# Kernel tuning notes

Measured on AMD Instinct MI355X. Metric: run time of the kernel, lower is better.

## Reference

```python
import math
import jax, jax.numpy as jnp
import numpy as np

WS = 8      # window_size
NT = 16     # n_theta
NR = 8      # n_r
PD = 32     # polar_proj_dim


def _polar_grid():
    # Matches LocalPolarPrior._build_polar_grid: [NR, NT, 2] with (x, y) in [-1, 1]
    radius = jnp.linspace(0.0, 1.0, NR)
    theta = jnp.linspace(0.0, 2.0 * math.pi, NT + 1)[:-1]
    rr, tt = jnp.meshgrid(radius, theta, indexing='ij')
    return jnp.stack([rr * jnp.cos(tt), rr * jnp.sin(tt)], axis=-1)


def _bilinear_weights():
    # Precompute flat gather indices + weights for F.grid_sample(mode='bilinear',
    # padding_mode='zeros', align_corners=True) on a fixed WSxWS input.
    g = _polar_grid()                                   # [NR, NT, 2]
    px = (g[..., 0] + 1.0) * 0.5 * (WS - 1)             # x -> pixel coords
    py = (g[..., 1] + 1.0) * 0.5 * (WS - 1)
    x0 = jnp.floor(px); y0 = jnp.floor(py)
    wx = px - x0; wy = py - y0
    xs = jnp.stack([x0, x0 + 1, x0, x0 + 1], axis=-1)   # [NR, NT, 4]
    ys = jnp.stack([y0, y0, y0 + 1, y0 + 1], axis=-1)
    ws = jnp.stack([(1 - wx) * (1 - wy), wx * (1 - wy),
                    (1 - wx) * wy, wx * wy], axis=-1)
    valid = (xs >= 0) & (xs < WS) & (ys >= 0) & (ys < WS)
    xi = jnp.clip(xs, 0, WS - 1).astype(jnp.int32)
    yi = jnp.clip(ys, 0, WS - 1).astype(jnp.int32)
    idx = (yi * WS + xi).reshape(NR * NT, 4)            # flat [0, 64)
    wt = (ws * valid).reshape(NR * NT, 4).astype(jnp.float32)
    return idx, wt


def setup_inputs() -> dict:
    key = jax.random.key(0)
    k1, k2, k3 = jax.random.split(key, 3)
    x = jax.random.normal(k1, (8, 96, 384, 384), jnp.float32)
    W_proj = jax.random.normal(k2, (PD, 96), jnp.float32) * 0.1
    b_proj = jax.random.normal(k3, (PD,), jnp.float32) * 0.1
    return {"x": x, "W_proj": W_proj, "b_proj": b_proj}


def reference(x, W_proj, b_proj):
    B, C, H, W = x.shape
    hg, wg = H // WS, W // WS
    # 1x1 conv projection
    feat = jnp.einsum('bchw,oc->bohw', x, W_proj) + b_proj[None, :, None, None]
    # window partition -> [B*hg*wg, PD, WS, WS]
    win = (feat.reshape(B, PD, hg, WS, wg, WS)
               .transpose(0, 2, 4, 1, 3, 5)
               .reshape(B * hg * wg, PD, WS, WS))
    # per-window orthonormal FFT2, shift, log-magnitude
    spec = jnp.fft.fftshift(jnp.fft.fft2(win, norm='ortho'), axes=(-2, -1))
    mag = jnp.log1p(jnp.abs(spec))                      # [N, PD, WS, WS]
    # fixed bilinear polar resample (data-independent weights)
    idx, wt = _bilinear_weights()                       # [NR*NT, 4]
    magf = mag.reshape(-1, PD, WS * WS)
    samp = magf[:, :, idx]                              # [N, PD, NR*NT, 4]
    polar = (samp * wt).sum(-1).reshape(-1, PD, NR, NT)
    # direction distribution per window
    logits = polar.mean(axis=(1, 2))                    # [N, NT]
    dist = jax.nn.softmax(logits, axis=-1)
    d_local = dist.reshape(B, hg, wg, NT).transpose(0, 3, 1, 2)
    entropy = -(d_local * jnp.log(jnp.clip(d_local, 1e-8))).sum(axis=1, keepdims=True)
    confidence = jnp.clip(1.0 - entropy / math.log(NT), 0.0, 1.0)
    return d_local.astype(x.dtype), confidence.astype(x.dtype)
```

## Files before the change

### kernel.cpp

```cpp
#include <hip/hip_runtime.h>
#include <hip/hip_bf16.h>
#include <math.h>

#define NT 16
#define NR 8
#define PD 32
#define HG 48
#define WG 48
#define NB 8
#define CH 96
#define HW 384
#define XHW (HW * HW)
#define S8 0.70710678118654752f

typedef short short8 __attribute__((ext_vector_type(8)));
typedef float f32x4 __attribute__((ext_vector_type(4)));

static __device__ const float CT16[16] = {
    1.0f, 0.9238795325112867f, 0.7071067811865476f, 0.3826834323650898f,
    0.0f, -0.3826834323650898f, -0.7071067811865476f, -0.9238795325112867f,
    -1.0f, -0.9238795325112867f, -0.7071067811865476f, -0.3826834323650898f,
    0.0f, 0.3826834323650898f, 0.7071067811865476f, 0.9238795325112867f};
static __device__ const float ST16[16] = {
    0.0f, 0.3826834323650898f, 0.7071067811865476f, 0.9238795325112867f,
    1.0f, 0.9238795325112867f, 0.7071067811865476f, 0.3826834323650898f,
    0.0f, -0.3826834323650898f, -0.7071067811865476f, -0.9238795325112867f,
    -1.0f, -0.9238795325112867f, -0.7071067811865476f, -0.3826834323650898f};

static __device__ __forceinline__ unsigned short f2bf(float f) {
  unsigned int u = __float_as_uint(f);
  u = u + 0x7fffu + ((u >> 16) & 1u);
  return (unsigned short)(u >> 16);
}
static __device__ __forceinline__ unsigned int pk2bf(float a, float b) {
  union { __hip_bfloat162 h; unsigned int u; } c;
  c.h = __float22bfloat162_rn(make_float2(a, b));
  return c.u;
}
static __device__ __forceinline__ float bf2f_lo(unsigned int v) {
  return __uint_as_float(v << 16);
}
static __device__ __forceinline__ float bf2f_hi(unsigned int v) {
  return __uint_as_float(v & 0xffff0000u);
}

#define MAGR(x_) log1pf(0.125f * fabsf(x_))
#define MAGC(re_, im_) log1pf(0.125f * sqrtf((re_) * (re_) + (im_) * (im_)))

__global__ void lpp_setup(const float* __restrict__ Wp,
                          unsigned short* __restrict__ ws) {
  int gt = blockIdx.x * 256 + threadIdx.x;
  if (gt < 384) {
    int f = gt >> 6, l = gt & 63;
    int ks = f >> 1, nt = f & 1;
    int n = nt * 16 + (l & 15);
    int kbase = ks * 32 + (l >> 4) * 8;
    for (int jj = 0; jj < 8; ++jj)
      ws[(f * 64 + l) * 8 + jj] = f2bf(Wp[n * CH + kbase + jj]);
  }
  if (gt >= 1024 && gt < 2048) {
    int q = gt - 1024;
    int j = q >> 4, t = q & 15;
    float g = 0.f;
    for (int r = 0; r < 8; ++r) {
      float rad = (float)r / 7.0f;
      float px = (rad * CT16[t] + 1.0f) * 3.5f;
      float py = (rad * ST16[t] + 1.0f) * 3.5f;
      float xf = floorf(px), yf = floorf(py);
      float wx = px - xf, wy = py - yf;
      int ix = (int)xf, iy = (int)yf;
      int xi0 = min(max(ix, 0), 7), xi1 = min(max(ix + 1, 0), 7);
      int yi0 = min(max(iy, 0), 7), yi1 = min(max(iy + 1, 0), 7);
      bool vx0 = (ix >= 0) && (ix < 8), vx1 = (ix + 1 >= 0) && (ix + 1 < 8);
      bool vy0 = (iy >= 0) && (iy < 8), vy1 = (iy + 1 >= 0) && (iy + 1 < 8);
      float w0 = (vx0 && vy0) ? (1.f - wx) * (1.f - wy) : 0.f;
      float w1 = (vx1 && vy0) ? wx * (1.f - wy) : 0.f;
      float w2 = (vx0 && vy1) ? (1.f - wx) * wy : 0.f;
      float w3 = (vx1 && vy1) ? wx * wy : 0.f;
      if (yi0 * 8 + xi0 == j) g += w0;
      if (yi0 * 8 + xi1 == j) g += w1;
      if (yi1 * 8 + xi0 == j) g += w2;
      if (yi1 * 8 + xi1 == j) g += w3;
    }
    int f = j >> 5, kc = (j >> 3) & 3, jj = j & 7;
    int l = (kc << 4) | t;
    ws[3072 + (f * 64 + l) * 8 + jj] = f2bf(g);
  }
}

__global__ __launch_bounds__(256, 4) void lpp_main(
    const float* __restrict__ x, const float* __restrict__ bp,
    const unsigned short* __restrict__ ws, float* __restrict__ out) {
  __shared__ short8 ldsX[2048];
  __shared__ float obuf[144];
  unsigned int* ldsU = (unsigned int*)ldsX;

  const int tid = threadIdx.x;
  const int lane = tid & 63;
  const int wave = tid >> 6;
  const int gid = blockIdx.x;
  const int wxg = gid % 6;
  const int hy = (gid / 6) % HG;
  const int b = gid / (6 * HG);
  const short8* wsV = (const short8*)ws;
  const int kcA = lane >> 4;

  f32x4 acc[8][2];
#pragma unroll
  for (int m = 0; m < 8; ++m) {
    acc[m][0] = (f32x4){0.f, 0.f, 0.f, 0.f};
    acc[m][1] = (f32x4){0.f, 0.f, 0.f, 0.f};
  }

  short8 bfr[6];
#pragma unroll
  for (int f = 0; f < 6; ++f) bfr[f] = wsV[f * 64 + lane];

  const int pw = wave * 128 + (lane & 15);
  const float* tb = x + (size_t)b * CH * XHW + (size_t)(hy * 8) * HW +
                    wxg * 64 + (size_t)(kcA * 8) * XHW;

  float lv[2][8];
#define LOADSTEP(DST, S)                                                     \
  {                                                                          \
    int px_ = pw + ((S) & 7) * 16;                                           \
    int pxo_ = (px_ >> 6) * HW + (px_ & 63);                                 \
    _Pragma("unroll") for (int j = 0; j < 8; ++j)                            \
        DST[j] = tb[(size_t)(((S) >> 3) * 32 + j) * XHW + pxo_];             \
  }

  LOADSTEP(lv[0], 0)
#pragma unroll
  for (int s = 0; s < 24; ++s) {
    if (s + 1 < 24) LOADSTEP(lv[(s + 1) & 1], s + 1)
    union { unsigned int u[4]; short8 v; } pk;
    pk.u[0] = pk2bf(lv[s & 1][0], lv[s & 1][1]);
    pk.u[1] = pk2bf(lv[s & 1][2], lv[s & 1][3]);
    pk.u[2] = pk2bf(lv[s & 1][4], lv[s & 1][5]);
    pk.u[3] = pk2bf(lv[s & 1][6], lv[s & 1][7]);
    acc[s & 7][0] = __builtin_amdgcn_mfma_f32_16x16x32_bf16(
        pk.v, bfr[(s >> 3) * 2 + 0], acc[s & 7][0], 0, 0, 0);
    acc[s & 7][1] = __builtin_amdgcn_mfma_f32_16x16x32_bf16(
        pk.v, bfr[(s >> 3) * 2 + 1], acc[s & 7][1], 0, 0, 0);
  }

  {
    const float bias0 = bp[lane & 15];
    const float bias1 = bp[16 + (lane & 15)];
    const int r_ = 2 * wave;
    const int c0 = ((lane >> 4) & 1) << 2;
    const int wb = (lane >> 5) & 1;
#pragma unroll
    for (int m = 0; m < 8; ++m) {
      int win = (2 * m + wb) & 7;
      int j0 = (r_ + (m >> 2)) * 8 + c0;
#pragma unroll
      for (int nt = 0; nt < 2; ++nt) {
        int p = win * 32 + nt * 16 + (lane & 15);
        float bs = nt ? bias1 : bias0;
        int sh = (p & 15) << 1;
        int dwb = p * 32;
        unsigned int w0 = pk2bf(acc[m][nt][0] + bs, acc[m][nt][1] + bs);
        unsigned int w1 = pk2bf(acc[m][nt][2] + bs, acc[m][nt][3] + bs);
        ldsU[dwb + ((j0 >> 1) ^ sh)] = w0;
        ldsU[dwb + (((j0 >> 1) + 1) ^ sh)] = w1;
      }
    }
  }
  __syncthreads();

  {
    const int p = tid;
    const int sh = (p & 15) << 1;
    const int dwb = p * 32;
    float rr[8][8];
#pragma unroll
    for (int k = 0; k < 8; ++k) {
      float v[8];
#pragma unroll
      for (int i = 0; i < 4; ++i) {
        unsigned int u = ldsU[dwb + ((k * 4 + i) ^ sh)];
        v[2 * i] = bf2f_lo(u);
        v[2 * i + 1] = bf2f_hi(u);
      }
      float a0 = v[0] + v[4], a1 = v[0] - v[4], a2 = v[2] + v[6], a3 = v[2] - v[6];
      float b0 = v[1] + v[5], b1 = v[1] - v[5], b2 = v[3] + v[7], b3 = v[3] - v[7];
      float e0 = a0 + a2, e2 = a0 - a2, o0 = b0 + b2, o2 = b0 - b2;
      float t1 = S8 * (b1 - b3), t2 = S8 * (b1 + b3);
      rr[k][0] = e0 + o0; rr[k][1] = e0 - o0;
      rr[k][2] = a1 + t1; rr[k][3] = -a3 - t2;
      rr[k][4] = e2;      rr[k][5] = -o2;
      rr[k][6] = a1 - t1; rr[k][7] = a3 - t2;
    }
    float mg0[5], mg4[5], mg1[8], mg2[8], mg3[8];
#define REALCOL(SLOT, OUT)                                                    \
  {                                                                           \
    float a0 = rr[0][SLOT] + rr[4][SLOT], a1 = rr[0][SLOT] - rr[4][SLOT];     \
    float a2 = rr[2][SLOT] + rr[6][SLOT], a3 = rr[2][SLOT] - rr[6][SLOT];     \
    float b0 = rr[1][SLOT] + rr[5][SLOT], b1 = rr[1][SLOT] - rr[5][SLOT];     \
    float b2 = rr[3][SLOT] + rr[7][SLOT], b3 = rr[3][SLOT] - rr[7][SLOT];     \
    float e0 = a0 + a2, e2 = a0 - a2, o0 = b0 + b2, o2 = b0 - b2;             \
    float t1 = S8 * (b1 - b3), t2 = S8 * (b1 + b3);                           \
    OUT[0] = MAGR(e0 + o0); OUT[4] = MAGR(e0 - o0);                           \
    OUT[1] = MAGC(a1 + t1, -a3 - t2);                                         \
    OUT[2] = MAGC(e2, -o2);                                                   \
    OUT[3] = MAGC(a1 - t1, a3 - t2);                                          \
  }
#define CPLXCOL(SR, SI, OUT)                                                  \
  {                                                                           \
    float t0r = rr[0][SR] + rr[4][SR], t0i = rr[0][SI] + rr[4][SI];           \
    float t1r = rr[0][SR] - rr[4][SR], t1i = rr[0][SI] - rr[4][SI];           \
    float t2r = rr[2][SR] + rr[6][SR], t2i = rr[2][SI] + rr[6][SI];           \
    float t3r = rr[2][SR] - rr[6][SR], t3i = rr[2][SI] - rr[6][SI];           \
    float E0r = t0r + t2r, E0i = t0i + t2i, E2r = t0r - t2r, E2i = t0i - t2i; \
    float E1r = t1r + t3i, E1i = t1i - t3r, E3r = t1r - t3i, E3i = t1i + t3r; \
    float u0r = rr[1][SR] + rr[5][SR], u0i = rr[1][SI] + rr[5][SI];           \
    float u1r = rr[1][SR] - rr[5][SR], u1i = rr[1][SI] - rr[5][SI];           \
    float u2r = rr[3][SR] + rr[7][SR], u2i = rr[3][SI] + rr[7][SI];           \
    float u3r = rr[3][SR] - rr[7][SR], u3i = rr[3][SI] - rr[7][SI];           \
    float O0r = u0r + u2r, O0i = u0i + u2i, O2r = u0r - u2r, O2i = u0i - u2i; \
    float O1r = u1r + u3i, O1i = u1i - u3r, O3r = u1r - u3i, O3i = u1i + u3r; \
    float W1r = S8 * (O1r + O1i), W1i = S8 * (O1i - O1r);                     \
    float W2r = O2i, W2i = -O2r;                                              \
    float W3r = S8 * (O3i - O3r), W3i = -S8 * (O3r + O3i);                    \
    OUT[0] = MAGC(E0r + O0r, E0i + O0i); OUT[4] = MAGC(E0r - O0r, E0i - O0i); \
    OUT[1] = MAGC(E1r + W1r, E1i + W1i); OUT[5] = MAGC(E1r - W1r, E1i - W1i); \
    OUT[2] = MAGC(E2r + W2r, E2i + W2i); OUT[6] = MAGC(E2r - W2r, E2i - W2i); \
    OUT[3] = MAGC(E3r + W3r, E3i + W3i); OUT[7] = MAGC(E3r - W3r, E3i - W3i); \
  }
    REALCOL(0, mg0)
    REALCOL(1, mg4)
    CPLXCOL(2, 3, mg1)
    CPLXCOL(4, 5, mg2)
    CPLXCOL(6, 7, mg3)
    const int pb8 = p * 8, p7 = p & 7;
#pragma unroll
    for (int up = 0; up < 8; ++up) {
      union { unsigned short h[8]; short8 v; } pk;
#pragma unroll
      for (int vp = 0; vp < 8; ++vp) {
        const int u = (up + 4) & 7, vx = (vp + 4) & 7;
        float m;
        if (vx == 0)      m = mg0[(u <= 4) ? u : (8 - u)];
        else if (vx == 4) m = mg4[(u <= 4) ? u : (8 - u)];
        else if (vx == 1) m = mg1[u];
        else if (vx == 2) m = mg2[u];
        else if (vx == 3) m = mg3[u];
        else { const int uu = (8 - u) & 7;
               m = (vx == 5) ? mg3[uu] : (vx == 6) ? mg2[uu] : mg1[uu]; }
        pk.h[vp] = f2bf(m);
      }
      ldsX[pb8 + (up ^ p7)] = pk.v;
    }
  }
  __syncthreads();

  {
    short8 gf0 = wsV[384 + lane];
    short8 gf1 = wsV[448 + lane];
    f32x4 ag[4];
#pragma unroll
    for (int pt = 0; pt < 4; ++pt) {
      int prow = (wave * 4 + pt) * 16 + (lane & 15);
      int p7 = prow & 7, pb = prow * 8;
      short8 a0 = ldsX[pb + (kcA ^ p7)];
      short8 a1 = ldsX[pb + ((kcA + 4) ^ p7)];
      f32x4 zf = (f32x4){0.f, 0.f, 0.f, 0.f};
      zf = __builtin_amdgcn_mfma_f32_16x16x32_bf16(a0, gf0, zf, 0, 0, 0);
      zf = __builtin_amdgcn_mfma_f32_16x16x32_bf16(a1, gf1, zf, 0, 0, 0);
      ag[pt] = zf;
    }
    float s0 = ag[0][0] + ag[0][1] + ag[0][2] + ag[0][3] +
               ag[1][0] + ag[1][1] + ag[1][2] + ag[1][3];
    float s1 = ag[2][0] + ag[2][1] + ag[2][2] + ag[2][3] +
               ag[3][0] + ag[3][1] + ag[3][2] + ag[3][3];
    s0 += __shfl_xor(s0, 16); s0 += __shfl_xor(s0, 32);
    s1 += __shfl_xor(s1, 16); s1 += __shfl_xor(s1, 32);
    float l0 = s0 * (1.0f / 256.0f), l1 = s1 * (1.0f / 256.0f);
    float m0 = l0, m1 = l1;
#pragma unroll
    for (int mk = 1; mk < 16; mk <<= 1) {
      m0 = fmaxf(m0, __shfl_xor(m0, mk));
      m1 = fmaxf(m1, __shfl_xor(m1, mk));
    }
    float e0 = expf(l0 - m0), e1 = expf(l1 - m1);
    float ss0 = e0, ss1 = e1;
#pragma unroll
    for (int mk = 1; mk < 16; mk <<= 1) {
      ss0 += __shfl_xor(ss0, mk);
      ss1 += __shfl_xor(ss1, mk);
    }
    float d0 = e0 / ss0, d1 = e1 / ss1;
    float h0 = -d0 * logf(fmaxf(d0, 1e-8f));
    float h1 = -d1 * logf(fmaxf(d1, 1e-8f));
#pragma unroll
    for (int mk = 1; mk < 16; mk <<= 1) {
      h0 += __shfl_xor(h0, mk);
      h1 += __shfl_xor(h1, mk);
    }
    float c0 = fminf(fmaxf(1.f - h0 * (1.0f / 2.7725887222397811f), 0.f), 1.f);
    float c1 = fminf(fmaxf(1.f - h1 * (1.0f / 2.7725887222397811f), 0.f), 1.f);
    if (lane < 16) {
      obuf[wave * 32 + lane] = d0;
      obuf[wave * 32 + 16 + lane] = d1;
    }
    if (lane == 0) {
      obuf[128 + wave * 2] = c0;
      obuf[128 + wave * 2 + 1] = c1;
    }
  }
  __syncthreads();

  if (tid < 128) {
    int t = tid >> 3, win = tid & 7;
    int wx = wxg * 8 + win;
    out[((size_t)(b * NT + t) * HG + hy) * WG + wx] = obuf[win * 16 + t];
  } else if (tid < 136) {
    int win = tid - 128;
    int wx = wxg * 8 + win;
    out[(size_t)NB * NT * HG * WG + ((size_t)b * HG + hy) * WG + wx] =
        obuf[128 + win];
  }
}

extern "C" void kernel_launch(void* const* d_in, const int* in_sizes, int n_in,
                              void* d_out, int out_size, void* d_ws,
                              size_t ws_size, hipStream_t stream) {
  (void)in_sizes; (void)n_in; (void)ws_size; (void)out_size;
  const float* x = (const float*)d_in[0];
  const float* Wp = (const float*)d_in[1];
  const float* bp = (const float*)d_in[2];
  unsigned short* ws = (unsigned short*)d_ws;
  float* out = (float*)d_out;
  lpp_setup<<<8, 256, 0, stream>>>(Wp, ws);
  lpp_main<<<NB * HG * 6, 256, 0, stream>>>(x, bp, ws, out);
}
```

Measured before the change: 137.7 us.

## Split fused projection+FFT kernel into separate projection and FFT kernels via workspace

Splits the single fused kernel into two. A projection kernel streams full 384-pixel rows of x through bf16 MFMA and writes the bias-added features to global workspace in bf16. A second kernel then reads those features per window and does the FFT, polar resample and softmax. The aim is more coalesced, row-contiguous reads of x and less register pressure per kernel. The cost is an extra global write and read of the intermediate feature map, about 75 MB in bf16, plus one more launch.

```diff
diff --git a/kernel.cpp b/kernel.cpp
--- a/kernel.cpp
+++ b/kernel.cpp
@@ -12,6 +12,7 @@
 #define HW 384
 #define XHW (HW * HW)
 #define S8 0.70710678118654752f
+#define FEAT0 8192
 
 typedef short short8 __attribute__((ext_vector_type(8)));
 typedef float f32x4 __attribute__((ext_vector_type(4)));
@@ -88,12 +89,81 @@
   }
 }
 
-__global__ __launch_bounds__(256, 4) void lpp_main(
+__global__ __launch_bounds__(256, 4) void lpp_proj(
     const float* __restrict__ x, const float* __restrict__ bp,
+    const unsigned short* __restrict__ wsc, unsigned short* __restrict__ wsf) {
+  const int tid = threadIdx.x;
+  const int lane = tid & 63;
+  const int l15 = lane & 15;
+  const int kcA = lane >> 4;
+  const int w = tid >> 6;
+  const int gid = blockIdx.x;
+  const int rh = gid & 1;
+  const int hy = (gid >> 1) % HG;
+  const int b = gid / (2 * HG);
+  const int R = hy * 8 + rh * 4 + w;
+  const int Rw = rh * 4 + w;
+  const short8* wsV = (const short8*)wsc;
+
+  short8 bfr[6];
+#pragma unroll
+  for (int f = 0; f < 6; ++f) bfr[f] = wsV[f * 64 + lane];
+  const float bs0 = bp[l15];
+  const float bs1 = bp[16 + l15];
+
+  const float* xr = x + (size_t)b * CH * XHW + (size_t)R * HW +
+                    (size_t)(kcA * 8) * XHW;
+  const int FB0 = FEAT0 + ((b * HG + hy) * 48 * 8 + Rw) * 256;
+  const int colw = (kcA & 1) << 2;
+  const int wsel = kcA >> 1;
+
+  float laA[24], laB[24];
+#define K1LOAD(DST, M)                                                       \
+  {                                                                          \
+    _Pragma("unroll") for (int ks = 0; ks < 3; ++ks)                         \
+        _Pragma("unroll") for (int j = 0; j < 8; ++j)                        \
+            DST[ks * 8 + j] =                                                \
+                xr[(size_t)(ks * 32 + j) * XHW + (M) * 16 + l15];            \
+  }
+#define K1BODY(CUR, NXT, M)                                                  \
+  {                                                                          \
+    if ((M) + 1 < 24) K1LOAD(NXT, (M) + 1);                                  \
+    f32x4 a0 = (f32x4){0.f, 0.f, 0.f, 0.f};                                  \
+    f32x4 a1 = (f32x4){0.f, 0.f, 0.f, 0.f};                                  \
+    _Pragma("unroll") for (int ks = 0; ks < 3; ++ks) {                       \
+      union { unsigned int u[4]; short8 v; } pk;                             \
+      pk.u[0] = pk2bf(CUR[ks * 8 + 0], CUR[ks * 8 + 1]);                     \
+      pk.u[1] = pk2bf(CUR[ks * 8 + 2], CUR[ks * 8 + 3]);                     \
+      pk.u[2] = pk2bf(CUR[ks * 8 + 4], CUR[ks * 8 + 5]);                     \
+      pk.u[3] = pk2bf(CUR[ks * 8 + 6], CUR[ks * 8 + 7]);                     \
+      a0 = __builtin_amdgcn_mfma_f32_16x16x32_bf16(pk.v, bfr[ks * 2 + 0],    \
+                                                   a0, 0, 0, 0);             \
+      a1 = __builtin_amdgcn_mfma_f32_16x16x32_bf16(pk.v, bfr[ks * 2 + 1],    \
+                                                   a1, 0, 0, 0);             \
+    }                                                                        \
+    int winR = 2 * (M) + wsel;                                               \
+    int ad0 = FB0 + winR * 2048 + l15 * 8 + colw;                            \
+    *(unsigned int*)&wsf[ad0] = pk2bf(a0[0] + bs0, a0[1] + bs0);             \
+    *(unsigned int*)&wsf[ad0 + 2] = pk2bf(a0[2] + bs0, a0[3] + bs0);         \
+    int ad1 = ad0 + 128;                                                     \
+    *(unsigned int*)&wsf[ad1] = pk2bf(a1[0] + bs1, a1[1] + bs1);             \
+    *(unsigned int*)&wsf[ad1 + 2] = pk2bf(a1[2] + bs1, a1[3] + bs1);         \
+  }
+
+  K1LOAD(laA, 0)
+#pragma unroll
+  for (int mm = 0; mm < 12; ++mm) {
+    K1BODY(laA, laB, 2 * mm)
+    K1BODY(laB, laA, 2 * mm + 1)
+  }
+#undef K1LOAD
+#undef K1BODY
+}
+
+__global__ __launch_bounds__(256, 4) void lpp_fft(
     const unsigned short* __restrict__ ws, float* __restrict__ out) {
   __shared__ short8 ldsX[2048];
   __shared__ float obuf[144];
-  unsigned int* ldsU = (unsigned int*)ldsX;
 
   const int tid = threadIdx.x;
   const int lane = tid & 63;
@@ -105,84 +175,23 @@
   const short8* wsV = (const short8*)ws;
   const int kcA = lane >> 4;
 
-  f32x4 acc[8][2];
-#pragma unroll
-  for (int m = 0; m < 8; ++m) {
-    acc[m][0] = (f32x4){0.f, 0.f, 0.f, 0.f};
-    acc[m][1] = (f32x4){0.f, 0.f, 0.f, 0.f};
-  }
-
-  short8 bfr[6];
-#pragma unroll
-  for (int f = 0; f < 6; ++f) bfr[f] = wsV[f * 64 + lane];
-
-  const int pw = wave * 128 + (lane & 15);
-  const float* tb = x + (size_t)b * CH * XHW + (size_t)(hy * 8) * HW +
-                    wxg * 64 + (size_t)(kcA * 8) * XHW;
-
-  float lv[2][8];
-#define LOADSTEP(DST, S)                                                     \
-  {                                                                          \
-    int px_ = pw + ((S) & 7) * 16;                                           \
-    int pxo_ = (px_ >> 6) * HW + (px_ & 63);                                 \
-    _Pragma("unroll") for (int j = 0; j < 8; ++j)                            \
-        DST[j] = tb[(size_t)(((S) >> 3) * 32 + j) * XHW + pxo_];             \
-  }
-
-  LOADSTEP(lv[0], 0)
-#pragma unroll
-  for (int s = 0; s < 24; ++s) {
-    if (s + 1 < 24) LOADSTEP(lv[(s + 1) & 1], s + 1)
-    union { unsigned int u[4]; short8 v; } pk;
-    pk.u[0] = pk2bf(lv[s & 1][0], lv[s & 1][1]);
-    pk.u[1] = pk2bf(lv[s & 1][2], lv[s & 1][3]);
-    pk.u[2] = pk2bf(lv[s & 1][4], lv[s & 1][5]);
-    pk.u[3] = pk2bf(lv[s & 1][6], lv[s & 1][7]);
-    acc[s & 7][0] = __builtin_amdgcn_mfma_f32_16x16x32_bf16(
-        pk.v, bfr[(s >> 3) * 2 + 0], acc[s & 7][0], 0, 0, 0);
-    acc[s & 7][1] = __builtin_amdgcn_mfma_f32_16x16x32_bf16(
-        pk.v, bfr[(s >> 3) * 2 + 1], acc[s & 7][1], 0, 0, 0);
-  }
-
   {
-    const float bias0 = bp[lane & 15];
-    const float bias1 = bp[16 + (lane & 15)];
-    const int r_ = 2 * wave;
-    const int c0 = ((lane >> 4) & 1) << 2;
-    const int wb = (lane >> 5) & 1;
-#pragma unroll
-    for (int m = 0; m < 8; ++m) {
-      int win = (2 * m + wb) & 7;
-      int j0 = (r_ + (m >> 2)) * 8 + c0;
-#pragma unroll
-      for (int nt = 0; nt < 2; ++nt) {
-        int p = win * 32 + nt * 16 + (lane & 15);
-        float bs = nt ? bias1 : bias0;
-        int sh = (p & 15) << 1;
-        int dwb = p * 32;
-        unsigned int w0 = pk2bf(acc[m][nt][0] + bs, acc[m][nt][1] + bs);
-        unsigned int w1 = pk2bf(acc[m][nt][2] + bs, acc[m][nt][3] + bs);
-        ldsU[dwb + ((j0 >> 1) ^ sh)] = w0;
-        ldsU[dwb + (((j0 >> 1) + 1) ^ sh)] = w1;
-      }
-    }
-  }
-  __syncthreads();
-
-  {
-    const int p = tid;
-    const int sh = (p & 15) << 1;
-    const int dwb = p * 32;
+    const int win8 = tid >> 5, o = tid & 31;
+    const int fbase =
+        FEAT0 + (((b * HG + hy) * 48 + wxg * 8 + win8) * 8) * 256 + o * 8;
+    uint4 fr[8];
+#pragma unroll
+    for (int r = 0; r < 8; ++r)
+      fr[r] = *(const uint4*)&ws[fbase + r * 256];
+
     float rr[8][8];
 #pragma unroll
     for (int k = 0; k < 8; ++k) {
       float v[8];
-#pragma unroll
-      for (int i = 0; i < 4; ++i) {
-        unsigned int u = ldsU[dwb + ((k * 4 + i) ^ sh)];
-        v[2 * i] = bf2f_lo(u);
-        v[2 * i + 1] = bf2f_hi(u);
-      }
+      v[0] = bf2f_lo(fr[k].x); v[1] = bf2f_hi(fr[k].x);
+      v[2] = bf2f_lo(fr[k].y); v[3] = bf2f_hi(fr[k].y);
+      v[4] = bf2f_lo(fr[k].z); v[5] = bf2f_hi(fr[k].z);
+      v[6] = bf2f_lo(fr[k].w); v[7] = bf2f_hi(fr[k].w);
       float a0 = v[0] + v[4], a1 = v[0] - v[4], a2 = v[2] + v[6], a3 = v[2] - v[6];
       float b0 = v[1] + v[5], b1 = v[1] - v[5], b2 = v[3] + v[7], b3 = v[3] - v[7];
       float e0 = a0 + a2, e2 = a0 - a2, o0 = b0 + b2, o2 = b0 - b2;
@@ -233,7 +242,7 @@
     CPLXCOL(2, 3, mg1)
     CPLXCOL(4, 5, mg2)
     CPLXCOL(6, 7, mg3)
-    const int pb8 = p * 8, p7 = p & 7;
+    const int pb8 = tid * 8, p7 = tid & 7;
 #pragma unroll
     for (int up = 0; up < 8; ++up) {
       union { unsigned short h[8]; short8 v; } pk;
@@ -333,5 +342,6 @@
   unsigned short* ws = (unsigned short*)d_ws;
   float* out = (float*)d_out;
   lpp_setup<<<8, 256, 0, stream>>>(Wp, ws);
-  lpp_main<<<NB * HG * 6, 256, 0, stream>>>(x, bp, ws, out);
-}
+  lpp_proj<<<NB * HG * 2, 256, 0, stream>>>(x, bp, ws, ws);
+  lpp_fft<<<NB * HG * 6, 256, 0, stream>>>(ws, out);
+}
```

Measured after the change: 331.2 us. 140% more time.
